# Optimization experiments

Hardware: AMD Instinct MI355X
Metric: run time of the kernel (lower is better)

The kernel has to match this reference:

```python
import jax, jax.numpy as jnp
import numpy as np

MROPE_SECTION = [16, 24, 24]
HEAD_DIM = 128
NUM_HEADS = 16
NUM_KV_HEADS = 8
EPS = 1e-6


def rmsnorm(x, w, eps=EPS):
    xf = x.astype(jnp.float32)
    var = jnp.mean(xf * xf, axis=-1, keepdims=True)
    return (w * (xf * jax.lax.rsqrt(var + eps))).astype(x.dtype)


def rotate_half(x):
    d = x.shape[-1] // 2
    return jnp.concatenate([-x[..., d:], x[..., :d]], axis=-1)


def build_mrope(c):
    # c: [3, B, S, head_dim]; pick modality i%3 per section (non-interleaved path)
    sec = MROPE_SECTION * 2
    splits = np.cumsum(sec)[:-1]
    parts = jnp.split(c, splits, axis=-1)
    out = jnp.concatenate([p[i % 3] for i, p in enumerate(parts)], axis=-1)  # [B,S,hd]
    return out[:, None]  # unsqueeze dim 1 -> [B,1,S,hd]


def setup_inputs() -> dict:
    key = jax.random.key(0)
    ks = jax.random.split(key, 8)
    B, S, D = 2, 2048, 2048
    hd, H, KV = HEAD_DIM, NUM_HEADS, NUM_KV_HEADS
    hidden_states = jax.random.normal(ks[0], (B, S, D), jnp.float32)
    cos = jax.random.uniform(ks[1], (3, B, S, hd), jnp.float32, -1.0, 1.0)
    sin = jax.random.uniform(ks[2], (3, B, S, hd), jnp.float32, -1.0, 1.0)
    # additive causal mask [B,1,S,S]
    neg = jnp.full((S, S), -1e9, jnp.float32)
    causal = jnp.triu(neg, k=1)
    attention_mask = jnp.broadcast_to(causal[None, None], (B, 1, S, S))
    sc = 0.02
    Wq = jax.random.normal(ks[3], (D, H * hd), jnp.float32) * sc
    Wk = jax.random.normal(ks[4], (D, KV * hd), jnp.float32) * sc
    Wv = jax.random.normal(ks[5], (D, KV * hd), jnp.float32) * sc
    Wo = jax.random.normal(ks[6], (H * hd, D), jnp.float32) * sc
    q_norm_w = jnp.ones((hd,), jnp.float32)
    k_norm_w = jnp.ones((hd,), jnp.float32)
    return dict(hidden_states=hidden_states, cos=cos, sin=sin,
                attention_mask=attention_mask, Wq=Wq, Wk=Wk, Wv=Wv, Wo=Wo,
                q_norm_w=q_norm_w, k_norm_w=k_norm_w)


def reference(hidden_states, cos, sin, attention_mask, Wq, Wk, Wv, Wo, q_norm_w, k_norm_w):
    B, S, D = hidden_states.shape
    hd, H, KV = HEAD_DIM, NUM_HEADS, NUM_KV_HEADS
    groups = H // KV
    scaling = hd ** -0.5

    q = (hidden_states @ Wq).reshape(B, S, H, hd)
    k = (hidden_states @ Wk).reshape(B, S, KV, hd)
    v = (hidden_states @ Wv).reshape(B, S, KV, hd)

    q = rmsnorm(q, q_norm_w).transpose(0, 2, 1, 3)  # [B,H,S,hd]
    k = rmsnorm(k, k_norm_w).transpose(0, 2, 1, 3)  # [B,KV,S,hd]
    v = v.transpose(0, 2, 1, 3)                      # [B,KV,S,hd]

    c = build_mrope(cos)  # [B,1,S,hd]
    s = build_mrope(sin)
    q = q * c + rotate_half(q) * s
    k = k * c + rotate_half(k) * s

    # repeat_kv (GQA)
    k = jnp.repeat(k, groups, axis=1)  # [B,H,S,hd]
    v = jnp.repeat(v, groups, axis=1)

    scores = jnp.einsum('bhqd,bhkd->bhqk', q, k) * scaling + attention_mask
    attn = jax.nn.softmax(scores.astype(jnp.float32), axis=-1).astype(q.dtype)
    out = jnp.einsum('bhqk,bhkd->bqhd', attn, v).reshape(B, S, H * hd)
    return out @ Wo
```

## Files before the change

### kernel.cpp

```cpp
#include <hip/hip_runtime.h>
#include <hip/hip_bf16.h>

typedef unsigned short u16;
typedef __bf16 bf16x8 __attribute__((ext_vector_type(8)));
typedef float f32x4 __attribute__((ext_vector_type(4)));

#define B_ 2
#define S_ 2048
#define SCALE_LOG2E 0.12751743f

static __device__ __forceinline__ u16 f2bf(float f) {
    union { float f; unsigned int u; } v; v.f = f;
    unsigned int r = v.u + 0x7fffu + ((v.u >> 16) & 1u);
    return (u16)(r >> 16);
}
static __device__ __forceinline__ float bf2f(unsigned int u) {
    union { unsigned int u; float f; } v; v.u = u << 16;
    return v.f;
}

__device__ __forceinline__ void gload16(const u16* g, u16* l) {
    __builtin_amdgcn_global_load_lds(
        (const __attribute__((address_space(1))) u16*)g,
        (__attribute__((address_space(3))) u16*)l,
        16, 0, 0);
}

__global__ __launch_bounds__(256) void cast_f32_bf16(const float* __restrict__ src,
                                                     u16* __restrict__ dst, int n4) {
    int i = blockIdx.x * 256 + threadIdx.x;
    if (i >= n4) return;
    float4 v = reinterpret_cast<const float4*>(src)[i];
    ushort4 o;
    o.x = f2bf(v.x); o.y = f2bf(v.y); o.z = f2bf(v.z); o.w = f2bf(v.w);
    reinterpret_cast<ushort4*>(dst)[i] = o;
}

__global__ __launch_bounds__(256) void transpose_cast(
    const float* __restrict__ src, u16* __restrict__ dst, int srs, int drs)
{
    __shared__ float tile[32][33];
    int c0 = blockIdx.x << 5, r0 = blockIdx.y << 5;
    int tx = threadIdx.x & 31, ty = threadIdx.x >> 5;
#pragma unroll
    for (int i = 0; i < 4; ++i)
        tile[ty + i * 8][tx] = src[(long long)(r0 + ty + i * 8) * srs + c0 + tx];
    __syncthreads();
#pragma unroll
    for (int i = 0; i < 4; ++i)
        dst[(long long)(c0 + ty + i * 8) * drs + r0 + tx] = f2bf(tile[tx][ty + i * 8]);
}

__global__ __launch_bounds__(256) void vtrans(const u16* __restrict__ src, u16* __restrict__ dst) {
    __shared__ u16 tile[32][34];
    int z = blockIdx.z;
    const u16* s = src + (size_t)(z >> 3) * 2048 * 4096 + 3072 + (z & 7) * 128;
    u16* d = dst + (size_t)z * 128 * 2048;
    int c0 = blockIdx.x << 5, r0 = blockIdx.y << 5;
    int tx = threadIdx.x & 31, ty = threadIdx.x >> 5;
#pragma unroll
    for (int i = 0; i < 4; ++i)
        tile[ty + i * 8][tx] = s[(size_t)(r0 + ty + i * 8) * 4096 + c0 + tx];
    __syncthreads();
#pragma unroll
    for (int i = 0; i < 4; ++i)
        d[(size_t)(c0 + ty + i * 8) * 2048 + r0 + tx] = tile[tx][ty + i * 8];
}

template<int BM, int BN, int OBF>
__global__ __launch_bounds__(256, 2) void gemm_tile(
    const u16* __restrict__ A, const u16* __restrict__ Bt,
    void* __restrict__ Cv, int M, int N, int K)
{
    constexpr int RM = BM / 32;
    constexpr int RN = BN / 32;
    constexpr int NGA = BM / 64;
    constexpr int NGB = BN / 64;
    __shared__ __align__(16) u16 As[BM * 32];
    __shared__ __align__(16) u16 Bs[BN * 32];
    int t = threadIdx.x;
    int wave = t >> 6, lane = t & 63;
    int quad = lane >> 4, l16 = lane & 15;
    int wm = (wave >> 1) * (BM / 2), wn = (wave & 1) * (BN / 2);
    int m0 = blockIdx.y * BM, n0 = blockIdx.x * BN;

    f32x4 acc[RM][RN];
#pragma unroll
    for (int i = 0; i < RM; ++i)
#pragma unroll
        for (int j = 0; j < RN; ++j)
            acc[i][j] = (f32x4){0.f, 0.f, 0.f, 0.f};

    int srow = wave * 16 + (lane >> 2);
    int sc8 = (lane & 3) << 3;
    const u16* Ap = A + (size_t)(m0 + srow) * K + sc8;
    const u16* Bp = Bt + (size_t)(n0 + srow) * K + sc8;
    size_t row64 = (size_t)64 * K;
    u16* lA = &As[(wave * 16) * 32];
    u16* lB = &Bs[(wave * 16) * 32];

    for (int k0 = 0; k0 < K; k0 += 32) {
#pragma unroll
        for (int g = 0; g < NGA; ++g)
            gload16(Ap + g * row64 + k0, lA + g * 64 * 32);
#pragma unroll
        for (int g = 0; g < NGB; ++g)
            gload16(Bp + g * row64 + k0, lB + g * 64 * 32);
        __syncthreads();
        bf16x8 af[RM], bfr[RN];
#pragma unroll
        for (int i = 0; i < RM; ++i)
            af[i] = *(const bf16x8*)(&As[(wm + i * 16 + l16) * 32 + quad * 8]);
#pragma unroll
        for (int j = 0; j < RN; ++j)
            bfr[j] = *(const bf16x8*)(&Bs[(wn + j * 16 + l16) * 32 + quad * 8]);
#pragma unroll
        for (int i = 0; i < RM; ++i)
#pragma unroll
            for (int j = 0; j < RN; ++j)
                acc[i][j] = __builtin_amdgcn_mfma_f32_16x16x32_bf16(af[i], bfr[j], acc[i][j], 0, 0, 0);
        __syncthreads();
    }

    if (OBF) {
        u16* C16 = (u16*)Cv;
#pragma unroll
        for (int i = 0; i < RM; ++i) {
            int rbase = m0 + wm + i * 16 + quad * 4;
#pragma unroll
            for (int j = 0; j < RN; ++j) {
                int col = n0 + wn + j * 16 + l16;
#pragma unroll
                for (int r = 0; r < 4; ++r)
                    C16[(size_t)(rbase + r) * N + col] = f2bf(acc[i][j][r]);
            }
        }
    } else {
        float* Cf = (float*)Cv;
#pragma unroll
        for (int i = 0; i < RM; ++i) {
            int rbase = m0 + wm + i * 16 + quad * 4;
#pragma unroll
            for (int j = 0; j < RN; ++j) {
                int col = n0 + wn + j * 16 + l16;
#pragma unroll
                for (int r = 0; r < 4; ++r)
                    Cf[(size_t)(rbase + r) * N + col] = acc[i][j][r];
            }
        }
    }
}

__global__ __launch_bounds__(256) void norm_rope(
    const u16* __restrict__ qkvb, const float* __restrict__ cosb,
    const float* __restrict__ sinb, const float* __restrict__ qw,
    const float* __restrict__ kw, u16* __restrict__ qout, u16* __restrict__ kout)
{
    int row = blockIdx.x;
    int b = row >> 11, s = row & 2047;
    int wave = threadIdx.x >> 6, lane = threadIdx.x & 63;
    int hv = blockIdx.y * 4 + wave;
    bool isq = hv < 16;
    int h = isq ? hv : hv - 16;
    const u16* src = qkvb + (size_t)row * 4096 + (isq ? h * 128 : 2048 + h * 128);
    int d0 = lane << 1;
    unsigned int xu = *(const unsigned int*)(src + d0);
    float x0 = bf2f(xu & 0xffffu), x1 = bf2f(xu >> 16);
    float ss = x0 * x0 + x1 * x1;
#pragma unroll
    for (int off = 32; off >= 1; off >>= 1) ss += __shfl_xor(ss, off);
    float rstd = rsqrtf(ss * (1.0f / 128.0f) + 1e-6f);
    const float* w = isq ? qw : kw;
    float2 wv = *(const float2*)(w + d0);
    float xn0 = x0 * rstd * wv.x;
    float xn1 = x1 * rstd * wv.y;
    float p0 = __shfl_xor(xn0, 32);
    float p1 = __shfl_xor(xn1, 32);
    float rh0 = (lane < 32) ? -p0 : p0;
    float rh1 = (lane < 32) ? -p1 : p1;
    int md = d0 < 16 ? 0 : d0 < 40 ? 1 : d0 < 64 ? 2 : d0 < 80 ? 0 : d0 < 104 ? 1 : 2;
    size_t cidx = ((size_t)md * (B_ * S_) + row) * 128 + d0;
    float2 c  = *(const float2*)(cosb + cidx);
    float2 sn = *(const float2*)(sinb + cidx);
    float fs = isq ? SCALE_LOG2E : 1.0f;
    float o0 = (xn0 * c.x + rh0 * sn.x) * fs;
    float o1 = (xn1 * c.y + rh1 * sn.y) * fs;
    size_t orow = isq ? ((size_t)(b * 16 + h) * 2048 + s) * 128
                      : ((size_t)(b * 8 + h) * 2048 + s) * 128;
    unsigned int pack = (unsigned int)f2bf(o0) | ((unsigned int)f2bf(o1) << 16);
    u16* dst = isq ? qout : kout;
    *(unsigned int*)(dst + orow + d0) = pack;
}

__global__ __launch_bounds__(256, 2) void attention(
    const u16* __restrict__ qb, const u16* __restrict__ kb,
    const u16* __restrict__ vt, u16* __restrict__ ao)
{
    __shared__ __align__(16) u16 Ks[2][64 * 128];
    __shared__ __align__(16) u16 Vs[2][128 * 64];
    __shared__ __align__(16) __bf16 Ps[4][2][16 * 64];

    int t = threadIdx.x;
    int wave = t >> 6, lane = t & 63;
    int quad = lane >> 4, l16 = lane & 15;
    int bx = blockIdx.x;
    int hi = bx >> 8, u = bx & 255;
    int q5 = u & 31;
    int qt = hi ? q5 : 31 - q5;
    int bkv = ((u >> 5) << 1) | hi;
    int b = bkv >> 3, kvh = bkv & 7;
    int q0 = qt << 6;

    bf16x8 af_q[2][4];
#pragma unroll
    for (int hh = 0; hh < 2; ++hh) {
        const u16* qsrc = qb + ((size_t)(b * 16 + kvh * 2 + hh) * 2048 + q0 + wave * 16 + l16) * 128 + quad * 8;
#pragma unroll
        for (int ks = 0; ks < 4; ++ks)
            af_q[hh][ks] = *(const bf16x8*)(qsrc + ks * 32);
    }

    const u16* kbase = kb + (size_t)bkv * 2048 * 128;
    const u16* vbase = vt + (size_t)bkv * 128 * 2048;
    const u16* kg[4]; const u16* vg[4];
    u16* kl0[4]; u16* kl1[4]; u16* vl0[4]; u16* vl1[4];
    {
        int kc = lane & 15, vc = lane & 7;
#pragma unroll
        for (int j = 0; j < 4; ++j) {
            int kr = wave * 16 + j * 4 + (lane >> 4);
            kg[j] = kbase + (size_t)kr * 128 + ((kc ^ (kr & 15)) << 3);
            int vr = wave * 32 + j * 8 + (lane >> 3);
            vg[j] = vbase + (size_t)vr * 2048 + ((vc ^ (vr & 7)) << 3);
            kl0[j] = &Ks[0][(wave * 16 + j * 4) * 128];
            kl1[j] = &Ks[1][(wave * 16 + j * 4) * 128];
            vl0[j] = &Vs[0][(wave * 32 + j * 8) * 64];
            vl1[j] = &Vs[1][(wave * 32 + j * 8) * 64];
        }
    }

    f32x4 o_acc[2][8];
    float lsum[2][4];
#pragma unroll
    for (int hh = 0; hh < 2; ++hh) {
#pragma unroll
        for (int i = 0; i < 8; ++i) o_acc[hh][i] = (f32x4){0.f, 0.f, 0.f, 0.f};
#pragma unroll
        for (int r = 0; r < 4; ++r) lsum[hh][r] = 0.f;
    }

#pragma unroll
    for (int j = 0; j < 4; ++j) { gload16(kg[j], kl0[j]); gload16(vg[j], vl0[j]); }

    for (int kt = 0; kt <= qt; ++kt) {
        int buf = kt & 1;
        __syncthreads();
        if (kt < qt) {
            size_t ko = (size_t)(kt + 1) * 64 * 128;
            int vo = (kt + 1) * 64;
            if (buf) {
#pragma unroll
                for (int j = 0; j < 4; ++j) { gload16(kg[j] + ko, kl0[j]); gload16(vg[j] + vo, vl0[j]); }
            } else {
#pragma unroll
                for (int j = 0; j < 4; ++j) { gload16(kg[j] + ko, kl1[j]); gload16(vg[j] + vo, vl1[j]); }
            }
        }
        const u16* Kb = Ks[buf];
        const u16* Vb = Vs[buf];

        f32x4 sa[2][4];
#pragma unroll
        for (int nt = 0; nt < 4; ++nt) { sa[0][nt] = (f32x4){0.f,0.f,0.f,0.f}; sa[1][nt] = (f32x4){0.f,0.f,0.f,0.f}; }
#pragma unroll
        for (int nt = 0; nt < 4; ++nt)
#pragma unroll
            for (int ks = 0; ks < 4; ++ks) {
                bf16x8 bk = *(const bf16x8*)(&Kb[(nt * 16 + l16) * 128 + ((((ks << 2) | quad) ^ l16) << 3)]);
                sa[0][nt] = __builtin_amdgcn_mfma_f32_16x16x32_bf16(af_q[0][ks], bk, sa[0][nt], 0, 0, 0);
                sa[1][nt] = __builtin_amdgcn_mfma_f32_16x16x32_bf16(af_q[1][ks], bk, sa[1][nt], 0, 0, 0);
            }

        bool diag = (kt == qt);
#pragma unroll
        for (int hh = 0; hh < 2; ++hh)
#pragma unroll
            for (int r = 0; r < 4; ++r) {
                int row = quad * 4 + r;
                int qi = wave * 16 + row;
#pragma unroll
                for (int nt = 0; nt < 4; ++nt) {
                    float pe = __builtin_amdgcn_exp2f(sa[hh][nt][r]);
                    int col = nt * 16 + l16;
                    if (diag && col > qi) pe = 0.f;
                    lsum[hh][r] += pe;
                    Ps[wave][hh][row * 64 + (col ^ ((row & 7) << 3))] = (__bf16)pe;
                }
            }

#pragma unroll
        for (int ks = 0; ks < 2; ++ks) {
            int csw = (((ks << 2) | quad) ^ (l16 & 7)) << 3;
            bf16x8 pa0 = *(const bf16x8*)(&Ps[wave][0][l16 * 64 + csw]);
            bf16x8 pa1 = *(const bf16x8*)(&Ps[wave][1][l16 * 64 + csw]);
#pragma unroll
            for (int dt = 0; dt < 8; ++dt) {
                bf16x8 vf = *(const bf16x8*)(&Vb[(dt * 16 + l16) * 64 + csw]);
                o_acc[0][dt] = __builtin_amdgcn_mfma_f32_16x16x32_bf16(pa0, vf, o_acc[0][dt], 0, 0, 0);
                o_acc[1][dt] = __builtin_amdgcn_mfma_f32_16x16x32_bf16(pa1, vf, o_acc[1][dt], 0, 0, 0);
            }
        }
    }

#pragma unroll
    for (int hh = 0; hh < 2; ++hh) {
#pragma unroll
        for (int r = 0; r < 4; ++r)
#pragma unroll
            for (int off = 1; off < 16; off <<= 1) lsum[hh][r] += __shfl_xor(lsum[hh][r], off);
        size_t obase = (((size_t)b * 2048 + q0 + wave * 16) * 16 + (kvh * 2 + hh)) * 128;
#pragma unroll
        for (int r = 0; r < 4; ++r) {
            float inv = 1.0f / lsum[hh][r];
            int qrow = quad * 4 + r;
#pragma unroll
            for (int dt = 0; dt < 8; ++dt)
                ao[obase + (size_t)qrow * 2048 + dt * 16 + l16] = f2bf(o_acc[hh][dt][r] * inv);
        }
    }
}

extern "C" void kernel_launch(void* const* d_in, const int* in_sizes, int n_in,
                              void* d_out, int out_size, void* d_ws, size_t ws_size,
                              hipStream_t stream) {
    const float* hs   = (const float*)d_in[0];
    const float* cosb = (const float*)d_in[1];
    const float* sinb = (const float*)d_in[2];
    const float* Wq = (const float*)d_in[4];
    const float* Wk = (const float*)d_in[5];
    const float* Wv = (const float*)d_in[6];
    const float* Wo = (const float*)d_in[7];
    const float* qw = (const float*)d_in[8];
    const float* kw = (const float*)d_in[9];
    float* out = (float*)d_out;

    char* ws = (char*)d_ws;
    u16* hsb   = (u16*)(ws);
    u16* wqkvb = (u16*)(ws + 16777216);
    u16* wob   = (u16*)(ws + 33554432);
    u16* qkvb  = (u16*)(ws + 41943040);
    u16* qb    = (u16*)(ws + 75497472);
    u16* kb    = (u16*)(ws + 92274688);
    u16* vb    = (u16*)(ws + 100663296);
    u16* aob   = (u16*)(ws + 109051904);

    cast_f32_bf16<<<8192, 256, 0, stream>>>(hs, hsb, 2097152);
    transpose_cast<<<dim3(64, 64), 256, 0, stream>>>(Wq, wqkvb,               2048, 2048);
    transpose_cast<<<dim3(32, 64), 256, 0, stream>>>(Wk, wqkvb + 2048 * 2048, 1024, 2048);
    transpose_cast<<<dim3(32, 64), 256, 0, stream>>>(Wv, wqkvb + 3072 * 2048, 1024, 2048);
    transpose_cast<<<dim3(64, 64), 256, 0, stream>>>(Wo, wob,                 2048, 2048);

    gemm_tile<256, 128, 1><<<dim3(32, 16), 256, 0, stream>>>(hsb, wqkvb, qkvb, 4096, 4096, 2048);

    norm_rope<<<dim3(4096, 6), 256, 0, stream>>>(qkvb, cosb, sinb, qw, kw, qb, kb);
    vtrans<<<dim3(4, 64, 16), 256, 0, stream>>>(qkvb, vb);

    attention<<<512, 256, 0, stream>>>(qb, kb, vb, aob);

    gemm_tile<256, 128, 0><<<dim3(16, 16), 256, 0, stream>>>(aob, wob, out, 4096, 2048, 2048);
}
```

Before: 397.9 us.

## Double-buffer GEMM LDS tiles and fuse vectorized weight transposes into one launch

The GEMM now ping-pongs between two LDS buffers. The next K-slice's global-to-LDS loads are issued right after a single barrier, so they overlap the MFMA work on the current slice, and the trailing barrier is gone. The four weight transpose-cast launches become one kernel that picks its source by block index and uses float4 reads with ushort4 writes. The V transpose is vectorized the same way. The cost is twice the GEMM shared memory, which may limit occupancy, and the correctness of the single barrier depends on it waiting for the async LDS loads to finish.

New measurement: 387.1 us. 2.7% less time.

```diff
diff --git a/kernel.cpp b/kernel.cpp
--- a/kernel.cpp
+++ b/kernel.cpp
@@ -36,35 +36,45 @@
     reinterpret_cast<ushort4*>(dst)[i] = o;
 }
 
-__global__ __launch_bounds__(256) void transpose_cast(
-    const float* __restrict__ src, u16* __restrict__ dst, int srs, int drs)
+__global__ __launch_bounds__(256) void wtrans_all(
+    const float* __restrict__ Wq, const float* __restrict__ Wk,
+    const float* __restrict__ Wv, const float* __restrict__ Wo,
+    u16* __restrict__ wqkvb, u16* __restrict__ wob)
 {
     __shared__ float tile[32][33];
-    int c0 = blockIdx.x << 5, r0 = blockIdx.y << 5;
-    int tx = threadIdx.x & 31, ty = threadIdx.x >> 5;
-#pragma unroll
-    for (int i = 0; i < 4; ++i)
-        tile[ty + i * 8][tx] = src[(long long)(r0 + ty + i * 8) * srs + c0 + tx];
+    int z = blockIdx.x;
+    const float* src; u16* dst; int srs, ct, zz;
+    if (z < 4096)      { src = Wq; dst = wqkvb;               srs = 2048; ct = 64; zz = z; }
+    else if (z < 6144) { src = Wk; dst = wqkvb + 2048 * 2048; srs = 1024; ct = 32; zz = z - 4096; }
+    else if (z < 8192) { src = Wv; dst = wqkvb + 3072 * 2048; srs = 1024; ct = 32; zz = z - 6144; }
+    else               { src = Wo; dst = wob;                 srs = 2048; ct = 64; zz = z - 8192; }
+    int c0 = (zz % ct) << 5, r0 = (zz / ct) << 5;
+    int t = threadIdx.x, tx = t & 7, ty = t >> 3;
+    float4 v = *(const float4*)&src[(size_t)(r0 + ty) * srs + c0 + 4 * tx];
+    tile[ty][4 * tx + 0] = v.x; tile[ty][4 * tx + 1] = v.y;
+    tile[ty][4 * tx + 2] = v.z; tile[ty][4 * tx + 3] = v.w;
     __syncthreads();
-#pragma unroll
-    for (int i = 0; i < 4; ++i)
-        dst[(long long)(c0 + ty + i * 8) * drs + r0 + tx] = f2bf(tile[tx][ty + i * 8]);
+    ushort4 o;
+    o.x = f2bf(tile[4 * tx + 0][ty]); o.y = f2bf(tile[4 * tx + 1][ty]);
+    o.z = f2bf(tile[4 * tx + 2][ty]); o.w = f2bf(tile[4 * tx + 3][ty]);
+    *(ushort4*)&dst[(size_t)(c0 + ty) * 2048 + r0 + 4 * tx] = o;
 }
 
 __global__ __launch_bounds__(256) void vtrans(const u16* __restrict__ src, u16* __restrict__ dst) {
-    __shared__ u16 tile[32][34];
+    __shared__ u16 tile[32][36];
     int z = blockIdx.z;
     const u16* s = src + (size_t)(z >> 3) * 2048 * 4096 + 3072 + (z & 7) * 128;
     u16* d = dst + (size_t)z * 128 * 2048;
     int c0 = blockIdx.x << 5, r0 = blockIdx.y << 5;
-    int tx = threadIdx.x & 31, ty = threadIdx.x >> 5;
-#pragma unroll
-    for (int i = 0; i < 4; ++i)
-        tile[ty + i * 8][tx] = s[(size_t)(r0 + ty + i * 8) * 4096 + c0 + tx];
+    int t = threadIdx.x, tx = t & 7, ty = t >> 3;
+    ushort4 v = *(const ushort4*)&s[(size_t)(r0 + ty) * 4096 + c0 + 4 * tx];
+    tile[ty][4 * tx + 0] = v.x; tile[ty][4 * tx + 1] = v.y;
+    tile[ty][4 * tx + 2] = v.z; tile[ty][4 * tx + 3] = v.w;
     __syncthreads();
-#pragma unroll
-    for (int i = 0; i < 4; ++i)
-        d[(size_t)(c0 + ty + i * 8) * 2048 + r0 + tx] = tile[tx][ty + i * 8];
+    ushort4 o;
+    o.x = tile[4 * tx + 0][ty]; o.y = tile[4 * tx + 1][ty];
+    o.z = tile[4 * tx + 2][ty]; o.w = tile[4 * tx + 3][ty];
+    *(ushort4*)&d[(size_t)(c0 + ty) * 2048 + r0 + 4 * tx] = o;
 }
 
 template<int BM, int BN, int OBF>
@@ -76,8 +86,8 @@
     constexpr int RN = BN / 32;
     constexpr int NGA = BM / 64;
     constexpr int NGB = BN / 64;
-    __shared__ __align__(16) u16 As[BM * 32];
-    __shared__ __align__(16) u16 Bs[BN * 32];
+    __shared__ __align__(16) u16 As[2][BM * 32];
+    __shared__ __align__(16) u16 Bs[2][BN * 32];
     int t = threadIdx.x;
     int wave = t >> 6, lane = t & 63;
     int quad = lane >> 4, l16 = lane & 15;
@@ -96,30 +106,37 @@
     const u16* Ap = A + (size_t)(m0 + srow) * K + sc8;
     const u16* Bp = Bt + (size_t)(n0 + srow) * K + sc8;
     size_t row64 = (size_t)64 * K;
-    u16* lA = &As[(wave * 16) * 32];
-    u16* lB = &Bs[(wave * 16) * 32];
-
-    for (int k0 = 0; k0 < K; k0 += 32) {
-#pragma unroll
-        for (int g = 0; g < NGA; ++g)
-            gload16(Ap + g * row64 + k0, lA + g * 64 * 32);
-#pragma unroll
-        for (int g = 0; g < NGB; ++g)
-            gload16(Bp + g * row64 + k0, lB + g * 64 * 32);
+    int lofs = (wave * 16) * 32;
+
+#pragma unroll
+    for (int g = 0; g < NGA; ++g) gload16(Ap + g * row64, &As[0][lofs + g * 64 * 32]);
+#pragma unroll
+    for (int g = 0; g < NGB; ++g) gload16(Bp + g * row64, &Bs[0][lofs + g * 64 * 32]);
+
+    int it = 0;
+    for (int k0 = 0; k0 < K; k0 += 32, ++it) {
+        int buf = it & 1;
         __syncthreads();
+        if (k0 + 32 < K) {
+            u16* dA = &As[buf ^ 1][lofs];
+            u16* dB = &Bs[buf ^ 1][lofs];
+#pragma unroll
+            for (int g = 0; g < NGA; ++g) gload16(Ap + g * row64 + k0 + 32, dA + g * 64 * 32);
+#pragma unroll
+            for (int g = 0; g < NGB; ++g) gload16(Bp + g * row64 + k0 + 32, dB + g * 64 * 32);
+        }
         bf16x8 af[RM], bfr[RN];
 #pragma unroll
         for (int i = 0; i < RM; ++i)
-            af[i] = *(const bf16x8*)(&As[(wm + i * 16 + l16) * 32 + quad * 8]);
+            af[i] = *(const bf16x8*)(&As[buf][(wm + i * 16 + l16) * 32 + quad * 8]);
 #pragma unroll
         for (int j = 0; j < RN; ++j)
-            bfr[j] = *(const bf16x8*)(&Bs[(wn + j * 16 + l16) * 32 + quad * 8]);
+            bfr[j] = *(const bf16x8*)(&Bs[buf][(wn + j * 16 + l16) * 32 + quad * 8]);
 #pragma unroll
         for (int i = 0; i < RM; ++i)
 #pragma unroll
             for (int j = 0; j < RN; ++j)
                 acc[i][j] = __builtin_amdgcn_mfma_f32_16x16x32_bf16(af[i], bfr[j], acc[i][j], 0, 0, 0);
-        __syncthreads();
     }
 
     if (OBF) {
@@ -355,10 +372,7 @@
     u16* aob   = (u16*)(ws + 109051904);
 
     cast_f32_bf16<<<8192, 256, 0, stream>>>(hs, hsb, 2097152);
-    transpose_cast<<<dim3(64, 64), 256, 0, stream>>>(Wq, wqkvb,               2048, 2048);
-    transpose_cast<<<dim3(32, 64), 256, 0, stream>>>(Wk, wqkvb + 2048 * 2048, 1024, 2048);
-    transpose_cast<<<dim3(32, 64), 256, 0, stream>>>(Wv, wqkvb + 3072 * 2048, 1024, 2048);
-    transpose_cast<<<dim3(64, 64), 256, 0, stream>>>(Wo, wob,                 2048, 2048);
+    wtrans_all<<<12288, 256, 0, stream>>>(Wq, Wk, Wv, Wo, wqkvb, wob);
 
     gemm_tile<256, 128, 1><<<dim3(32, 16), 256, 0, stream>>>(hsb, wqkvb, qkvb, 4096, 4096, 2048);
 
```
